# Performance work log

Measured on AMD Instinct MI355X. Metric: run time of the kernel, lower is better.

Reference implementation:

```python
import jax, jax.numpy as jnp
from jax import lax
import numpy as np

SR = 48000
NUM_BANDS = 12
IR_LEN = 32768          # reverb impulse-response length in samples
NUM_TAPS = 511          # bandpass FIR length for the noise filterbank
BS, CHS, T = 32, 2, 131072
EPS = 1e-8


def make_filterbank():
    """12-band windowed-sinc bandpass filterbank spanning 0..Nyquist."""
    n = np.arange(NUM_TAPS) - (NUM_TAPS - 1) / 2.0
    win = np.hamming(NUM_TAPS)
    filts = []
    for b in range(NUM_BANDS):
        lo = 0.5 * b / NUM_BANDS
        hi = 0.5 * (b + 1) / NUM_BANDS
        h = 2.0 * hi * np.sinc(2.0 * hi * n) - 2.0 * lo * np.sinc(2.0 * lo * n)
        filts.append(h * win)
    return np.stack(filts).astype(np.float32)  # (12, NUM_TAPS)


def _distortion(x, drive_db):
    # tanh waveshaper with dB drive gain
    return jnp.tanh(x * 10.0 ** (drive_db / 20.0))


def _compressor(x, thr, ratio, atk_ms, rel_ms, knee, makeup):
    # soft-knee gain computer in dB domain
    x_db = 20.0 * jnp.log10(jnp.abs(x) + EPS)          # (bs, chs, T)
    knee = jnp.maximum(knee, 1e-3)
    over = x_db - thr
    g_knee = x_db + (1.0 / ratio - 1.0) * (over + knee / 2.0) ** 2 / (2.0 * knee)
    g = jnp.where(2.0 * over < -knee, x_db,
                  jnp.where(2.0 * over > knee, thr + over / ratio, g_knee))
    gain_db = g - x_db                                  # desired gain reduction (<= 0)
    # per-sample attack/release one-pole envelope follower (sequential scan)
    alpha_a = jnp.exp(-1.0 / (SR * atk_ms / 1000.0))
    alpha_r = jnp.exp(-1.0 / (SR * rel_ms / 1000.0))
    g_t = jnp.moveaxis(gain_db, -1, 0)                  # (T, bs, chs)

    def step(prev, cur):
        alpha = jnp.where(cur < prev, alpha_a, alpha_r)  # attack when reduction grows
        new = alpha * prev + (1.0 - alpha) * cur
        return new, new

    _, smooth = lax.scan(step, jnp.zeros(g_t.shape[1:], x.dtype), g_t)
    smooth = jnp.moveaxis(smooth, 0, -1)                # (bs, chs, T)
    return x * 10.0 ** ((smooth + makeup) / 20.0)


def _reverb(x, band_gains, band_decays, mix, noise, fir_bank):
    bs, chs, seq = x.shape
    n = noise.reshape(bs * chs, NUM_BANDS, -1)          # (N, 12, IR_LEN+TAPS-1)
    # grouped conv: each band of noise filtered by its bandpass FIR
    filt = lax.conv_general_dilated(
        n, fir_bank[:, None, :], (1,), 'VALID',
        dimension_numbers=('NCH', 'OIH', 'NCH'),
        feature_group_count=NUM_BANDS)                  # (N, 12, IR_LEN)
    t = jnp.linspace(0.0, 1.0, IR_LEN, dtype=x.dtype)
    d = band_decays * 10.0 + 1.0
    env = jnp.exp(-d[:, None] * t[None, :])             # (12, IR_LEN) decay envelopes
    ir = jnp.mean(filt * (env * band_gains[:, None]), axis=1)  # (N, IR_LEN)
    ir = ir.reshape(bs, chs, IR_LEN)
    # FFT convolution of input with the synthesized IR
    nfft = seq + IR_LEN - 1
    wet = jnp.fft.irfft(jnp.fft.rfft(x, nfft) * jnp.fft.rfft(ir, nfft), nfft)[..., :seq]
    return (1.0 - mix) * x + mix * wet


def _forward(x, drive, thr, ratio, atk, rel, knee, makeup, mix,
             band_gains, band_decays, noise, fir_bank):
    x = _distortion(x, drive)
    x = _compressor(x, thr, ratio, atk, rel, knee, makeup)
    return _reverb(x, band_gains, band_decays, mix, noise, fir_bank)


def setup_inputs() -> dict:
    key = jax.random.key(0)
    k1, k2 = jax.random.split(key)
    return {
        "x": 0.5 * jax.random.normal(k1, (BS, CHS, T), jnp.float32),
        "drive": jnp.float32(5.0),
        "threshold_db": jnp.float32(-20.0),
        "ratio": jnp.float32(4.0),
        "attack_ms": jnp.float32(10.0),
        "release_ms": jnp.float32(50.0),
        "knee_db": jnp.float32(6.0),
        "makeup_gain_db": jnp.float32(0.0),
        "mix": jnp.float32(0.3),
        "band_gains": jnp.zeros((NUM_BANDS,), jnp.float32),
        "band_decays": 0.5 * jnp.ones((NUM_BANDS,), jnp.float32),
        "noise": jax.random.normal(k2, (BS, CHS, NUM_BANDS, IR_LEN + NUM_TAPS - 1), jnp.float32),
        "fir_bank": jnp.asarray(make_filterbank()),
    }


def reference(x, drive, threshold_db, ratio, attack_ms, release_ms, knee_db,
              makeup_gain_db, mix, band_gains, band_decays, noise, fir_bank):
    return _forward(x, drive, threshold_db, ratio, attack_ms, release_ms,
                    knee_db, makeup_gain_db, mix, band_gains, band_decays,
                    noise, fir_bank)
```

## Files before the change

### kernel.cpp

```cpp
#include <hip/hip_runtime.h>
#include <math.h>
#include <stdint.h>

#define NCHW    64
#define TLEN    131072
#define IRLEN   32768
#define NTAPS   511
#define NBANDS  12
#define NOISELEN (IRLEN + NTAPS - 1)

#define WUP     4096
#define CHK     512
#define NBLK2   (TLEN / CHK)
#define NQ      (TLEN / 4)
#define GRP     16

#define K10     0.16609640474436813f
#define DB2     6.0205999132796239f

__device__ __forceinline__ float fast_tanh(float z) {
    float az = fabsf(z);
    float e  = exp2f(az * 2.8853900817779268f);
    float r  = 1.0f - 2.0f / (e + 1.0f);
    return copysignf(r, z);
}

__device__ __forceinline__ float gain_db_one(float xs, float g, float thr,
                                             float q, float knee, float inv2k) {
    float y    = fast_tanh(xs * g);
    float a    = fabsf(y) + 1e-8f;
    float xdb  = __log2f(a) * DB2;
    float over = xdb - thr;
    float h    = over + 0.5f * knee;
    float gk   = q * h * h * inv2k;
    float t2   = 2.0f * over;
    return (t2 < -knee) ? 0.0f : ((t2 > knee) ? q * over : gk);
}

__device__ __forceinline__ float f4c(const float4& v, int s) {
    return s == 0 ? v.x : (s == 1 ? v.y : (s == 2 ? v.z : v.w));
}

__global__ __launch_bounds__(256) void k1_gain(
    const float* __restrict__ x,
    const float* __restrict__ p_drive, const float* __restrict__ p_thr,
    const float* __restrict__ p_ratio, const float* __restrict__ p_knee,
    const float* __restrict__ p_atk,   const float* __restrict__ p_rel,
    const float* __restrict__ band_gains,
    float4* __restrict__ q4, float* __restrict__ q1, float4* __restrict__ pq,
    int* __restrict__ flag)
{
    if (blockIdx.x == 0 && threadIdx.x == 0) {
        int f = 0;
        #pragma unroll
        for (int b = 0; b < NBANDS; ++b) f |= (band_gains[b] != 0.0f) ? 1 : 0;
        *flag = f;
    }
    __shared__ float S[64 * 65];
    int t0 = blockIdx.x * 64;
    int l  = threadIdx.x & 63;
    int w  = threadIdx.x >> 6;

    float g     = exp2f(p_drive[0] * K10);
    float thr   = p_thr[0];
    float knee  = fmaxf(p_knee[0], 1e-3f);
    float qr    = 1.0f / p_ratio[0] - 1.0f;
    float inv2k = 1.0f / (2.0f * knee);
    float aa    = expf(-1.0f / (48.0f * p_atk[0]));
    float ar    = expf(-1.0f / (48.0f * p_rel[0]));
    float omaa  = 1.0f - aa;
    float rho   = (1.0f - ar) / omaa;

    #pragma unroll
    for (int i = 0; i < 16; ++i) {
        int ch = w * 16 + i;
        float xv = x[(size_t)ch * TLEN + t0 + l];
        S[l * 65 + ch] = omaa * gain_db_one(xv, g, thr, qr, knee, inv2k);
    }
    __syncthreads();

    int ch = threadIdx.x & 63;
    int ql = threadIdx.x >> 6;
    #pragma unroll
    for (int k = 0; k < 4; ++k) {
        int qq = ql * 4 + k;
        int sb = qq * 4;
        float A0 = S[(sb + 0) * 65 + ch];
        float A1 = S[(sb + 1) * 65 + ch];
        float A2 = S[(sb + 2) * 65 + ch];
        float A3 = S[(sb + 3) * 65 + ch];
        float R0 = rho * A0, R1 = rho * A1, R2 = rho * A2, R3 = rho * A3;
        float i0 = A0, i1 = R0;
        float n0 = fmaf(aa, i0, A1);
        float n1 = fminf(fmaf(aa, i1, A1), fmaf(ar, i0, R1));
        float n2 = fmaf(ar, i1, R1);
        float m0 = fmaf(aa, n0, A2);
        float m1 = fminf(fmaf(aa, n1, A2), fmaf(ar, n0, R2));
        float m2 = fminf(fmaf(aa, n2, A2), fmaf(ar, n1, R2));
        float m3 = fmaf(ar, n2, R2);
        float o0 = fmaf(aa, m0, A3);
        float o1 = fminf(fmaf(aa, m1, A3), fmaf(ar, m0, R3));
        float o2 = fminf(fmaf(aa, m2, A3), fmaf(ar, m1, R3));
        float o3 = fminf(fmaf(aa, m3, A3), fmaf(ar, m2, R3));
        float o4 = fmaf(ar, m3, R3);
        size_t gi = (size_t)(blockIdx.x * 16 + qq) * 64 + ch;
        q4[gi] = make_float4(o0, o1, o2, o3);
        q1[gi] = o4;
        pq[gi] = make_float4(A0, A1, A2, A3);
    }
}

#define WSTEP(c4, c1s) { \
    float f0 = fmaf(s0, p, (c4).x); \
    float f1 = fmaf(s1, p, (c4).y); \
    float f2 = fmaf(s2, p, (c4).z); \
    float f3 = fmaf(s3, p, (c4).w); \
    float f4 = fmaf(s4, p, (c1s)); \
    p = fminf(fminf(fminf(f0, f1), f2), fminf(f3, f4)); \
}

#define ESTEP(Av, tl) { \
    float fa = fmaf(aa, p, (Av)); \
    float fr = fmaf(ar, p, rho * (Av)); \
    p = fminf(fa, fr); \
    Ssm[(tl) * 68 + lane] = p; \
}

#define APPLY(xv, tq, cq) { \
    float4 sm0 = *(const float4*)&Ssm[(4 * (tq) + 0) * 68 + (cq) * 4]; \
    float4 sm1 = *(const float4*)&Ssm[(4 * (tq) + 1) * 68 + (cq) * 4]; \
    float4 sm2 = *(const float4*)&Ssm[(4 * (tq) + 2) * 68 + (cq) * 4]; \
    float4 sm3 = *(const float4*)&Ssm[(4 * (tq) + 3) * 68 + (cq) * 4]; \
    _Pragma("unroll") \
    for (int cc = 0; cc < 4; ++cc) { \
        float c0 = fast_tanh(f4c(xv[cc], 0) * g) * exp2f((f4c(sm0, cc) + mk) * K10); \
        float c1 = fast_tanh(f4c(xv[cc], 1) * g) * exp2f((f4c(sm1, cc) + mk) * K10); \
        float c2 = fast_tanh(f4c(xv[cc], 2) * g) * exp2f((f4c(sm2, cc) + mk) * K10); \
        float c3 = fast_tanh(f4c(xv[cc], 3) * g) * exp2f((f4c(sm3, cc) + mk) * K10); \
        size_t oidx = (size_t)((cq) * 4 + cc) * TLEN + tb + 4 * (tq); \
        *(float4*)&out[oidx] = make_float4(dry * c0, dry * c1, dry * c2, dry * c3); \
        if (sflag) *(float4*)&comp[oidx] = make_float4(c0, c1, c2, c3); \
    } \
}

__global__ __launch_bounds__(256, 1) void k2_env(
    const float* __restrict__ x,
    const float4* __restrict__ q4, const float* __restrict__ q1,
    const float4* __restrict__ pq,
    const float* __restrict__ p_atk, const float* __restrict__ p_rel,
    const float* __restrict__ p_drive, const float* __restrict__ p_makeup,
    const float* __restrict__ p_mix, const int* __restrict__ flag,
    float* __restrict__ out, float* __restrict__ comp)
{
    __shared__ __attribute__((aligned(16))) float Ssm[128 * 68];
    __shared__ int sflag;
    int tid = threadIdx.x;
    if (tid == 0) sflag = *flag;

    int b  = blockIdx.x;
    int j  = ((b & 7) << 5) | (b >> 3);
    int te = j * CHK;
    int t0 = (j >= WUP / CHK) ? te - WUP : 0;
    int q0 = t0 >> 2, qe = te >> 2;
    int lane = tid & 63;

    float aa  = expf(-1.0f / (48.0f * p_atk[0]));
    float ar  = expf(-1.0f / (48.0f * p_rel[0]));
    float rho = (1.0f - ar) / (1.0f - aa);
    float s0 = aa * aa * aa * aa, s1 = aa * aa * aa * ar, s2 = aa * aa * ar * ar,
          s3 = aa * ar * ar * ar, s4 = ar * ar * ar * ar;
    float g   = exp2f(p_drive[0] * K10);
    float mk  = p_makeup[0];
    float mix = p_mix[0];
    float dry = 1.0f - mix;

    float p = 0.0f;

    if (tid < 64 && qe > q0) {
        float4 A4[GRP]; float A1v[GRP]; float4 B4[GRP]; float B1v[GRP];
        size_t base = (size_t)q0 * 64 + lane;
        #pragma unroll
        for (int u = 0; u < GRP; ++u) {
            A4[u]  = q4[base + (size_t)u * 64];
            A1v[u] = q1[base + (size_t)u * 64];
        }
        for (int gq = q0; gq < qe; gq += 2 * GRP) {
            size_t bb = (size_t)(gq + GRP) * 64 + lane;
            #pragma unroll
            for (int u = 0; u < GRP; ++u) {
                B4[u]  = q4[bb + (size_t)u * 64];
                B1v[u] = q1[bb + (size_t)u * 64];
            }
            #pragma unroll
            for (int u = 0; u < GRP; ++u) WSTEP(A4[u], A1v[u]);
            size_t ab = (size_t)(gq + 2 * GRP) * 64 + lane;
            #pragma unroll
            for (int u = 0; u < GRP; ++u) {
                A4[u]  = q4[ab + (size_t)u * 64];
                A1v[u] = q1[ab + (size_t)u * 64];
            }
            #pragma unroll
            for (int u = 0; u < GRP; ++u) WSTEP(B4[u], B1v[u]);
        }
    }

    int tqa = tid & 31,         cqa = tid >> 5;
    int tqb = (tid + 256) & 31, cqb = (tid + 256) >> 5;

    for (int r = 0; r < 4; ++r) {
        int tb = te + r * 128;
        float4 xva[4], xvb[4];
        #pragma unroll
        for (int cc = 0; cc < 4; ++cc) {
            xva[cc] = *(const float4*)&x[(size_t)(cqa * 4 + cc) * TLEN + tb + 4 * tqa];
            xvb[cc] = *(const float4*)&x[(size_t)(cqb * 4 + cc) * TLEN + tb + 4 * tqb];
        }
        if (tid < 64) {
            float4 C4[GRP], D4[GRP];
            size_t eb = (size_t)(qe + r * 32) * 64 + lane;
            #pragma unroll
            for (int u = 0; u < GRP; ++u) C4[u] = pq[eb + (size_t)u * 64];
            #pragma unroll
            for (int u = 0; u < GRP; ++u) D4[u] = pq[eb + (size_t)(u + GRP) * 64];
            #pragma unroll
            for (int u = 0; u < GRP; ++u) {
                ESTEP(C4[u].x, u * 4 + 0); ESTEP(C4[u].y, u * 4 + 1);
                ESTEP(C4[u].z, u * 4 + 2); ESTEP(C4[u].w, u * 4 + 3);
            }
            #pragma unroll
            for (int u = 0; u < GRP; ++u) {
                int t4 = (u + GRP) * 4;
                ESTEP(D4[u].x, t4 + 0); ESTEP(D4[u].y, t4 + 1);
                ESTEP(D4[u].z, t4 + 2); ESTEP(D4[u].w, t4 + 3);
            }
        }
        __syncthreads();
        APPLY(xva, tqa, cqa);
        APPLY(xvb, tqb, cqb);
        __syncthreads();
    }
}

__global__ __launch_bounds__(256) void k4_ir(
    const float* __restrict__ noise, const float* __restrict__ fir,
    const float* __restrict__ gains, const float* __restrict__ decays,
    const int* __restrict__ flag, float* __restrict__ ir)
{
    __shared__ int sflag;
    if (threadIdx.x == 0) sflag = *flag;
    __syncthreads();
    if (!sflag) return;
    __shared__ float sf[NBANDS * NTAPS];
    for (int i = threadIdx.x; i < NBANDS * NTAPS; i += 256) sf[i] = fir[i];
    __syncthreads();
    size_t total  = (size_t)NCHW * IRLEN;
    size_t stride = (size_t)gridDim.x * 256;
    for (size_t idx = blockIdx.x * 256 + threadIdx.x; idx < total; idx += stride) {
        int nch = (int)(idx >> 15);
        int n   = (int)(idx & (IRLEN - 1));
        float tl  = n * (1.0f / (IRLEN - 1));
        float acc = 0.0f;
        for (int bb = 0; bb < NBANDS; ++bb) {
            float gb = gains[bb];
            if (gb == 0.0f) continue;
            float env = expf(-(decays[bb] * 10.0f + 1.0f) * tl) * gb;
            const float* np_ = noise + ((size_t)nch * NBANDS + bb) * NOISELEN + n;
            const float* fb  = sf + bb * NTAPS;
            float s = 0.0f;
            for (int k = 0; k < NTAPS; ++k) s = fmaf(np_[k], fb[k], s);
            acc = fmaf(env, s, acc);
        }
        ir[idx] = acc * (1.0f / NBANDS);
    }
}

__global__ __launch_bounds__(256) void k5_wet(
    const float* __restrict__ comp, const float* __restrict__ ir,
    const float* __restrict__ p_mix, const int* __restrict__ flag,
    float* __restrict__ out)
{
    __shared__ int sflag;
    if (threadIdx.x == 0) sflag = *flag;
    __syncthreads();
    if (!sflag) return;
    float mix = p_mix[0];
    size_t total  = (size_t)NCHW * TLEN;
    size_t stride = (size_t)gridDim.x * 256;
    for (size_t idx = blockIdx.x * 256 + threadIdx.x; idx < total; idx += stride) {
        int nch = (int)(idx >> 17);
        int t   = (int)(idx & (TLEN - 1));
        const float* c   = comp + (size_t)nch * TLEN;
        const float* irp = ir + (size_t)nch * IRLEN;
        int kmax = (t < IRLEN - 1) ? t : (IRLEN - 1);
        float s = 0.0f;
        for (int k = 0; k <= kmax; ++k) s = fmaf(irp[k], c[t - k], s);
        out[idx] += mix * s;
    }
}

extern "C" void kernel_launch(void* const* d_in, const int* in_sizes, int n_in,
                              void* d_out, int out_size, void* d_ws, size_t ws_size,
                              hipStream_t stream)
{
    const float* x      = (const float*)d_in[0];
    const float* drive  = (const float*)d_in[1];
    const float* thr    = (const float*)d_in[2];
    const float* ratio  = (const float*)d_in[3];
    const float* atk    = (const float*)d_in[4];
    const float* rel    = (const float*)d_in[5];
    const float* knee   = (const float*)d_in[6];
    const float* makeup = (const float*)d_in[7];
    const float* mix    = (const float*)d_in[8];
    const float* bg     = (const float*)d_in[9];
    const float* bd     = (const float*)d_in[10];
    const float* noise  = (const float*)d_in[11];
    const float* fir    = (const float*)d_in[12];
    float* out = (float*)d_out;

    char*  w    = (char*)d_ws;
    int*   flag = (int*)w;
    float* q4f  = (float*)(w + 16);
    float* q1f  = q4f + (size_t)NQ * 256;
    float* pqf  = q1f + (size_t)NQ * 64;
    float* cmp  = pqf + (size_t)NQ * 256;
    float* ir   = cmp + (size_t)NCHW * TLEN;

    k1_gain<<<TLEN / 64, 256, 0, stream>>>(x, drive, thr, ratio, knee, atk, rel,
                                           bg, (float4*)q4f, q1f, (float4*)pqf, flag);
    k2_env<<<NBLK2, 256, 0, stream>>>(x, (const float4*)q4f, q1f, (const float4*)pqf,
                                      atk, rel, drive, makeup, mix, flag, out, cmp);
    k4_ir<<<256, 256, 0, stream>>>(noise, fir, bg, bd, flag, ir);
    k5_wet<<<256, 256, 0, stream>>>(cmp, ir, mix, flag, out);
}
```

Measured before the change: 253.3 us.

## Use idle waves to prefetch warm-up scan data into L2 via LDS loads

In the envelope warm-up scan only wave 0 does work. The three idle waves now issue global_load_lds requests two iterations ahead into a throwaway LDS buffer, so the q4/q1 lines are already in cache when wave 0 reads them. Each iteration ends with an s_barrier to keep the waves in step. The aim is to hide the latency of the serial scan's global loads, at the cost of extra memory traffic and a barrier per iteration.

Result: slower. 272.0 us (+7.4%).

```diff
diff --git a/kernel.cpp b/kernel.cpp
--- a/kernel.cpp
+++ b/kernel.cpp
@@ -153,6 +153,7 @@
     float* __restrict__ out, float* __restrict__ comp)
 {
     __shared__ __attribute__((aligned(16))) float Ssm[128 * 68];
+    __shared__ __attribute__((aligned(16))) char  Pdump[3 * 1024];
     __shared__ int sflag;
     int tid = threadIdx.x;
     if (tid == 0) sflag = *flag;
@@ -163,6 +164,7 @@
     int t0 = (j >= WUP / CHK) ? te - WUP : 0;
     int q0 = t0 >> 2, qe = te >> 2;
     int lane = tid & 63;
+    int wv   = tid >> 6;
 
     float aa  = expf(-1.0f / (48.0f * p_atk[0]));
     float ar  = expf(-1.0f / (48.0f * p_rel[0]));
@@ -175,34 +177,60 @@
     float dry = 1.0f - mix;
 
     float p = 0.0f;
-
-    if (tid < 64 && qe > q0) {
+    int nit = (qe - q0) >> 5;
+
+    if (nit > 0) {
         float4 A4[GRP]; float A1v[GRP]; float4 B4[GRP]; float B1v[GRP];
-        size_t base = (size_t)q0 * 64 + lane;
-        #pragma unroll
-        for (int u = 0; u < GRP; ++u) {
-            A4[u]  = q4[base + (size_t)u * 64];
-            A1v[u] = q1[base + (size_t)u * 64];
-        }
-        for (int gq = q0; gq < qe; gq += 2 * GRP) {
-            size_t bb = (size_t)(gq + GRP) * 64 + lane;
+        if (wv == 0) {
+            size_t base = (size_t)q0 * 64 + lane;
             #pragma unroll
             for (int u = 0; u < GRP; ++u) {
-                B4[u]  = q4[bb + (size_t)u * 64];
-                B1v[u] = q1[bb + (size_t)u * 64];
+                A4[u]  = q4[base + (size_t)u * 64];
+                A1v[u] = q1[base + (size_t)u * 64];
             }
-            #pragma unroll
-            for (int u = 0; u < GRP; ++u) WSTEP(A4[u], A1v[u]);
-            size_t ab = (size_t)(gq + 2 * GRP) * 64 + lane;
-            #pragma unroll
-            for (int u = 0; u < GRP; ++u) {
-                A4[u]  = q4[ab + (size_t)u * 64];
-                A1v[u] = q1[ab + (size_t)u * 64];
+        }
+        for (int it = 0; it < nit; ++it) {
+            if (wv == 0) {
+                int gq = q0 + it * 32;
+                size_t bb = (size_t)(gq + GRP) * 64 + lane;
+                #pragma unroll
+                for (int u = 0; u < GRP; ++u) {
+                    B4[u]  = q4[bb + (size_t)u * 64];
+                    B1v[u] = q1[bb + (size_t)u * 64];
+                }
+                #pragma unroll
+                for (int u = 0; u < GRP; ++u) WSTEP(A4[u], A1v[u]);
+                size_t ab = (size_t)(gq + 2 * GRP) * 64 + lane;
+                #pragma unroll
+                for (int u = 0; u < GRP; ++u) {
+                    A4[u]  = q4[ab + (size_t)u * 64];
+                    A1v[u] = q1[ab + (size_t)u * 64];
+                }
+                #pragma unroll
+                for (int u = 0; u < GRP; ++u) WSTEP(B4[u], B1v[u]);
+            } else {
+                int qp = q0 + (it + 2) * 32;
+                if (qp < qe) {
+                    char* dsink = Pdump + (wv - 1) * 1024;
+                    #pragma unroll
+                    for (int i_ = 0; i_ < 14; ++i_) {
+                        int rr = (wv - 1) + 3 * i_;
+                        if (rr < 40) {
+                            const char* sp = (rr < 32)
+                                ? (const char*)q4 + (((size_t)(qp + rr)) << 10) + lane * 16
+                                : (const char*)q1 + (((size_t)(qp + 4 * (rr - 32))) << 8) + lane * 16;
+                            __builtin_amdgcn_global_load_lds(
+                                (const __attribute__((address_space(1))) void*)sp,
+                                (__attribute__((address_space(3))) void*)dsink, 16, 0, 0);
+                        }
+                    }
+                }
             }
-            #pragma unroll
-            for (int u = 0; u < GRP; ++u) WSTEP(B4[u], B1v[u]);
-        }
-    }
+            __builtin_amdgcn_s_barrier();
+        }
+        if (wv != 0) asm volatile("s_waitcnt vmcnt(0)" ::: "memory");
+    }
+    __syncthreads();
 
     int tqa = tid & 31,         cqa = tid >> 5;
     int tqb = (tid + 256) & 31, cqb = (tid + 256) >> 5;
@@ -216,20 +244,20 @@
             xvb[cc] = *(const float4*)&x[(size_t)(cqb * 4 + cc) * TLEN + tb + 4 * tqb];
         }
         if (tid < 64) {
-            float4 C4[GRP], D4[GRP];
+            float4 C4[16], D4[16];
             size_t eb = (size_t)(qe + r * 32) * 64 + lane;
             #pragma unroll
-            for (int u = 0; u < GRP; ++u) C4[u] = pq[eb + (size_t)u * 64];
-            #pragma unroll
-            for (int u = 0; u < GRP; ++u) D4[u] = pq[eb + (size_t)(u + GRP) * 64];
-            #pragma unroll
-            for (int u = 0; u < GRP; ++u) {
+            for (int u = 0; u < 16; ++u) C4[u] = pq[eb + (size_t)u * 64];
+            #pragma unroll
+            for (int u = 0; u < 16; ++u) D4[u] = pq[eb + (size_t)(u + 16) * 64];
+            #pragma unroll
+            for (int u = 0; u < 16; ++u) {
                 ESTEP(C4[u].x, u * 4 + 0); ESTEP(C4[u].y, u * 4 + 1);
                 ESTEP(C4[u].z, u * 4 + 2); ESTEP(C4[u].w, u * 4 + 3);
             }
             #pragma unroll
-            for (int u = 0; u < GRP; ++u) {
-                int t4 = (u + GRP) * 4;
+            for (int u = 0; u < 16; ++u) {
+                int t4 = (u + 16) * 4;
                 ESTEP(D4[u].x, t4 + 0); ESTEP(D4[u].y, t4 + 1);
                 ESTEP(D4[u].z, t4 + 2); ESTEP(D4[u].w, t4 + 3);
             }
```
